# Performance work log

Measured on AMD Instinct MI355X. Metric: run time of the kernel, lower is better.

## Reference

```python
import jax, jax.numpy as jnp
import numpy as np

B, S, C, H = 256, 512, 64, 128  # batch, seq_len, input channels, LSTM hidden


def setup_inputs() -> dict:
    key = jax.random.key(0)
    ks = jax.random.split(key, 9)
    s = 1.0 / np.sqrt(H)  # torch nn.LSTM init: U(-1/sqrt(H), 1/sqrt(H))
    u = lambda k, shape: jax.random.uniform(k, shape, jnp.float32, -s, s)
    return {
        "x": jax.random.normal(ks[0], (B, S, C), jnp.float32),
        # layer 0 (input size C)
        "Wih0": u(ks[1], (4 * H, C)),
        "Whh0": u(ks[2], (4 * H, H)),
        "bih0": u(ks[3], (4 * H,)),
        "bhh0": u(ks[4], (4 * H,)),
        # layer 1 (input size H)
        "Wih1": u(ks[5], (4 * H, H)),
        "Whh1": u(ks[6], (4 * H, H)),
        "bih1": u(ks[7], (4 * H,)),
        "bhh1": u(ks[8], (4 * H,)),
    }


def _lstm_layer(x, Wih, Whh, bih, bhh):
    """x: (S, B, in) -> outputs h_t for all t: (S, B, H). Torch gate order i,f,g,o."""
    Hh = Whh.shape[1]
    # Input-to-hidden GEMM hoisted out of the recurrence (batched over S).
    xg = jnp.einsum('sbc,gc->sbg', x, Wih) + bih + bhh  # (S, B, 4H)

    def step(carry, xt):
        h, c = carry
        g = xt + h @ Whh.T  # (B, 4H)
        i, f, gg, o = jnp.split(g, 4, axis=-1)
        i = jax.nn.sigmoid(i)
        f = jax.nn.sigmoid(f)
        gg = jnp.tanh(gg)
        o = jax.nn.sigmoid(o)
        c = f * c + i * gg
        h = o * jnp.tanh(c)
        return (h, c), h

    h0 = jnp.zeros((x.shape[1], Hh), x.dtype)
    _, ys = jax.lax.scan(step, (h0, h0), xg)
    return ys


def reference(x, Wih0, Whh0, bih0, bhh0, Wih1, Whh1, bih1, bhh1):
    xs = jnp.transpose(x, (1, 0, 2))  # (B,S,C) -> (S,B,C), matching x.permute(1,0,2)
    y1 = _lstm_layer(xs, Wih0, Whh0, bih0, bhh0)
    y2 = _lstm_layer(y1, Wih1, Whh1, bih1, bhh1)
    return y2[-1]  # x[-1, :, :]: last timestep of top layer, (B, H)
```

## Files before the change

kernel.cpp:

```cpp
#include <hip/hip_runtime.h>
#include <cstdint>
#include <cstddef>


#define S_LEN 512
#define B_SZ  256
#define C_IN  64
#define HDIM  128
#define XG_TSTRIDE (32 * 512 * 8)

using short8  = __attribute__((ext_vector_type(8))) short;
using float4v = __attribute__((ext_vector_type(4))) float;

template<bool V> struct Flag { static constexpr bool value = V; };

__device__ __forceinline__ unsigned short f2b(float f) {
    union { float f; unsigned int u; } v; v.f = f;
    unsigned int u = v.u;
    return (unsigned short)((u + 0x7FFFu + ((u >> 16) & 1u)) >> 16);
}
__device__ __forceinline__ float b2f(unsigned short s) {
    union { unsigned int u; float f; } v; v.u = ((unsigned int)s) << 16;
    return v.f;
}
__device__ __forceinline__ float sig_(float x) {
    return __builtin_amdgcn_rcpf(1.0f + __builtin_amdgcn_exp2f(x * -1.442695041f));
}
__device__ __forceinline__ float tanh_(float x) {
    return 1.0f - 2.0f * __builtin_amdgcn_rcpf(1.0f + __builtin_amdgcn_exp2f(x * 2.885390082f));
}
__device__ __forceinline__ short8 load8_f2b(const float* s) {
    const float4v f0 = *(const float4v*)s;
    const float4v f1 = *(const float4v*)(s + 4);
    short8 t;
#pragma unroll
    for (int e = 0; e < 4; ++e) {
        t[e]     = (short)f2b(f0[e]);
        t[e + 4] = (short)f2b(f1[e]);
    }
    return t;
}

__global__ void conv_kernel(const float* __restrict__ whh0,
                            const float* __restrict__ wih1, const float* __restrict__ whh1,
                            const float* __restrict__ bih1, const float* __restrict__ bhh1,
                            unsigned short* __restrict__ whh0_b, unsigned short* __restrict__ wih1_b,
                            unsigned short* __restrict__ whh1_b, float* __restrict__ bias1) {
    int i = blockIdx.x * blockDim.x + threadIdx.x;
    if (i < 4 * HDIM * HDIM) {
        whh0_b[i] = f2b(whh0[i]);
        wih1_b[i] = f2b(wih1[i]);
        whh1_b[i] = f2b(whh1[i]);
    }
    if (i < 4 * HDIM) bias1[i] = bih1[i] + bhh1[i];
}

__global__ __launch_bounds__(512, 2)
void xg_gemm(const float* __restrict__ x, const float* __restrict__ wih0,
             const float* __restrict__ bih0, const float* __restrict__ bhh0,
             unsigned short* __restrict__ xg) {
    const int tid = threadIdx.x;
    const int w = tid >> 6, L = tid & 63, q = L >> 4, r = L & 15;
    const int blk = blockIdx.x, tch = blockIdx.y;
    const int boff = blk * 8, j = w * 16 + r;
    const int rowload = (r >> 2) * 2 + (r & 1);

    short8 wf[4][2]; float bias_s[4];
#pragma unroll
    for (int g = 0; g < 4; ++g) {
        const int nrow = g * HDIM + j;
#pragma unroll
        for (int kk = 0; kk < 2; ++kk)
            wf[g][kk] = load8_f2b(wih0 + (size_t)nrow * C_IN + kk * 32 + q * 8);
        bias_s[g] = bih0[nrow] + bhh0[nrow];
    }

    const float* px = x + ((size_t)(boff + rowload) * S_LEN + (size_t)tch * 32) * C_IN + q * 8;
    unsigned short* po = xg + ((size_t)(tch * 32) * 32 + blk) * 4096 + (size_t)tid * 8;

    for (int tt = 0; tt < 32; ++tt) {
        short8 xa[2];
#pragma unroll
        for (int kk = 0; kk < 2; ++kk) xa[kk] = load8_f2b(px + kk * 32);
        float4v a[4];
#pragma unroll
        for (int g = 0; g < 4; ++g) a[g] = (float4v){bias_s[g], bias_s[g], 0.f, 0.f};
#pragma unroll
        for (int kk = 0; kk < 2; ++kk)
#pragma unroll
            for (int g = 0; g < 4; ++g)
                a[g] = __builtin_amdgcn_mfma_f32_16x16x32_bf16(xa[kk], wf[g][kk], a[g], 0, 0, 0);
        short8 o;
#pragma unroll
        for (int g = 0; g < 4; ++g) {
            o[2 * g]     = (short)f2b(a[g][0]);
            o[2 * g + 1] = (short)f2b(a[g][1]);
        }
        *(short8*)po = o;
        px += C_IN;
        po += XG_TSTRIDE;
    }
}

__global__ __launch_bounds__(512, 2)
void lstm_fused(const unsigned short* __restrict__ whh0_b,
                const unsigned short* __restrict__ wih1_b,
                const unsigned short* __restrict__ whh1_b,
                const float* __restrict__ bias1,
                const unsigned short* __restrict__ xg,
                float* __restrict__ out) {
    __shared__ __align__(16) unsigned short hbuf[4 * 2048];
    const int tid = threadIdx.x;
    const int w = tid >> 6, L = tid & 63, q = L >> 4, r = L & 15;
    const int blk = blockIdx.x;
    const int boff = blk * 8, j = w * 16 + r;

    short8 whh0[4][4], wih1[4][4], whh1[4][4];
    float b1s[4];
#pragma unroll
    for (int g = 0; g < 4; ++g) {
        const size_t nrow = (size_t)(g * HDIM + j);
#pragma unroll
        for (int kk = 0; kk < 4; ++kk) {
            whh0[g][kk] = *(const short8*)(whh0_b + nrow * HDIM + kk * 32 + q * 8);
            wih1[g][kk] = *(const short8*)(wih1_b + nrow * HDIM + kk * 32 + q * 8);
            whh1[g][kk] = *(const short8*)(whh1_b + nrow * HDIM + kk * 32 + q * 8);
        }
        b1s[g] = bias1[g * HDIM + j];
    }
#pragma unroll
    for (int g = 0; g < 4; ++g) {
        asm volatile("" : "+v"(whh0[g][0]), "+v"(whh0[g][1]), "+v"(whh0[g][2]), "+v"(whh0[g][3]));
        asm volatile("" : "+v"(wih1[g][0]), "+v"(wih1[g][1]), "+v"(wih1[g][2]), "+v"(wih1[g][3]));
        asm volatile("" : "+v"(whh1[g][0]), "+v"(whh1[g][1]), "+v"(whh1[g][2]), "+v"(whh1[g][3]));
    }

    for (int idx = tid; idx < 4 * 1024; idx += 512) ((unsigned int*)hbuf)[idx] = 0u;

    float cf0[2] = {0.f, 0.f}, cf1[2] = {0.f, 0.f};
    const int rred = ((r & 3) < 2) ? r : (r - 2);
    const int rdoff = q * 128 + rred * 8;
    const int chunkbase = (j >> 3) * 128 + (j & 7);
    float* fout = out + (size_t)(boff + 2 * q) * HDIM + j;

    const unsigned short* pxg = xg + (size_t)blk * 4096 + (size_t)tid * 8;
    short8 xgA = *(const short8*)pxg;
    pxg += XG_TSTRIDE;
    short8 xgB;

    __syncthreads();

    auto step = [&](auto D0_, auto D1_, auto FIN_,
                    unsigned short* r0, unsigned short* w0,
                    unsigned short* r1, unsigned short* w1,
                    short8& xc, short8& xn) {
        constexpr bool D0  = decltype(D0_)::value;
        constexpr bool D1  = decltype(D1_)::value;
        constexpr bool FIN = decltype(FIN_)::value;

        if constexpr (!FIN) {
            xn = *(const short8*)pxg;
            pxg += XG_TSTRIDE;
        }

        if constexpr (D0) {
            float4v a0[4];
#pragma unroll
            for (int g = 0; g < 4; ++g)
                a0[g] = (float4v){b2f((unsigned short)xc[2 * g]),
                                  b2f((unsigned short)xc[2 * g + 1]), 0.f, 0.f};
#pragma unroll
            for (int kk = 0; kk < 4; ++kk) {
                const short8 h0f = *(const short8*)(r0 + kk * 512 + rdoff);
#pragma unroll
                for (int g = 0; g < 4; ++g)
                    a0[g] = __builtin_amdgcn_mfma_f32_16x16x32_bf16(h0f, whh0[g][kk], a0[g], 0, 0, 0);
            }
#pragma unroll
            for (int rr = 0; rr < 2; ++rr) {
                const float iv = sig_(a0[0][rr]);
                const float fv = sig_(a0[1][rr]);
                const float gv = tanh_(a0[2][rr]);
                const float ov = sig_(a0[3][rr]);
                cf0[rr] = fv * cf0[rr] + iv * gv;
                w0[chunkbase + (4 * q + rr) * 8] = f2b(ov * tanh_(cf0[rr]));
            }
        }

        if constexpr (D1) {
            float4v a1[4];
#pragma unroll
            for (int g = 0; g < 4; ++g) a1[g] = (float4v){b1s[g], b1s[g], 0.f, 0.f};
#pragma unroll
            for (int kk = 0; kk < 4; ++kk) {
                const short8 hif = *(const short8*)(r0 + kk * 512 + rdoff);
#pragma unroll
                for (int g = 0; g < 4; ++g)
                    a1[g] = __builtin_amdgcn_mfma_f32_16x16x32_bf16(hif, wih1[g][kk], a1[g], 0, 0, 0);
            }
#pragma unroll
            for (int kk = 0; kk < 4; ++kk) {
                const short8 h1f = *(const short8*)(r1 + kk * 512 + rdoff);
#pragma unroll
                for (int g = 0; g < 4; ++g)
                    a1[g] = __builtin_amdgcn_mfma_f32_16x16x32_bf16(h1f, whh1[g][kk], a1[g], 0, 0, 0);
            }
#pragma unroll
            for (int rr = 0; rr < 2; ++rr) {
                const float iv = sig_(a1[0][rr]);
                const float fv = sig_(a1[1][rr]);
                const float gv = tanh_(a1[2][rr]);
                const float ov = sig_(a1[3][rr]);
                cf1[rr] = fv * cf1[rr] + iv * gv;
                const float hv = ov * tanh_(cf1[rr]);
                if constexpr (FIN) fout[rr * HDIM] = hv;
                else w1[chunkbase + (4 * q + rr) * 8] = f2b(hv);
            }
        }

        if constexpr (!FIN)
            asm volatile("s_waitcnt lgkmcnt(0)\n\ts_barrier" ::: "memory");
    };

    unsigned short* h0A = hbuf;
    unsigned short* h0B = hbuf + 2048;
    unsigned short* h1A = hbuf + 4096;
    unsigned short* h1B = hbuf + 6144;
    using T = Flag<true>; using F = Flag<false>;

    step(T{}, F{}, F{}, h0A, h0B, h1A, h1B, xgA, xgB);
#pragma unroll 1
    for (int k = 0; k < 255; ++k) {
        step(T{}, T{}, F{}, h0B, h0A, h1B, h1A, xgB, xgA);
        step(T{}, T{}, F{}, h0A, h0B, h1A, h1B, xgA, xgB);
    }
    step(T{}, T{}, F{}, h0B, h0A, h1B, h1A, xgB, xgA);
    step(F{}, T{}, T{}, h0A, h0B, h1A, h1B, xgA, xgB);
}


extern "C" void kernel_launch(void* const* d_in, const int* in_sizes, int n_in,
                              void* d_out, int out_size, void* d_ws, size_t ws_size,
                              hipStream_t stream) {
    const float* x    = (const float*)d_in[0];
    const float* wih0 = (const float*)d_in[1];
    const float* whh0 = (const float*)d_in[2];
    const float* bih0 = (const float*)d_in[3];
    const float* bhh0 = (const float*)d_in[4];
    const float* wih1 = (const float*)d_in[5];
    const float* whh1 = (const float*)d_in[6];
    const float* bih1 = (const float*)d_in[7];
    const float* bhh1 = (const float*)d_in[8];

    char* ws = (char*)d_ws;
    unsigned short* whh0_b = (unsigned short*)(ws + 0);
    unsigned short* wih1_b = (unsigned short*)(ws + 131072);
    unsigned short* whh1_b = (unsigned short*)(ws + 262144);
    float*          bias1  = (float*)(ws + 393216);
    unsigned short* xgp    = (unsigned short*)(ws + 524288);

    conv_kernel<<<256, 256, 0, stream>>>(whh0, wih1, whh1, bih1, bhh1,
                                         whh0_b, wih1_b, whh1_b, bias1);
    xg_gemm<<<dim3(32, 16), 512, 0, stream>>>(x, wih0, bih0, bhh0, xgp);
    lstm_fused<<<32, 512, 0, stream>>>(whh0_b, wih1_b, whh1_b, bias1, xgp,
                                       (float*)d_out);
}
```

Measured before the change: 738.7 us.

## Halve per-block batch to 4 rows and launch 64 blocks; add MFMA priority

Each block of the fused LSTM kernel and the xg GEMM now handles 4 batch rows instead of 8, doubling the grid from 32 to 64 blocks, so more CUs work on the serial recurrence. The xg layout changes to match: 4 gate values per thread stored as short4. Each thread now computes one output row instead of two, which shortens the elementwise gate tail per step. s_setprio is raised around the MFMA chains. The cost is that MFMA tiles are now only 1/4 used, and the weight loads into registers are duplicated across twice as many blocks.

Result: faster. 694.5 us (-6.0%).

```diff
diff --git a/kernel.cpp b/kernel.cpp
--- a/kernel.cpp
+++ b/kernel.cpp
@@ -7,8 +7,10 @@
 #define B_SZ  256
 #define C_IN  64
 #define HDIM  128
-#define XG_TSTRIDE (32 * 512 * 8)
-
+#define NBLK  64
+#define XG_TSTRIDE (64 * 512 * 4)
+
+using short4v = __attribute__((ext_vector_type(4))) short;
 using short8  = __attribute__((ext_vector_type(8))) short;
 using float4v = __attribute__((ext_vector_type(4))) float;
 
@@ -62,8 +64,8 @@
     const int tid = threadIdx.x;
     const int w = tid >> 6, L = tid & 63, q = L >> 4, r = L & 15;
     const int blk = blockIdx.x, tch = blockIdx.y;
-    const int boff = blk * 8, j = w * 16 + r;
-    const int rowload = (r >> 2) * 2 + (r & 1);
+    const int boff = blk * 4, j = w * 16 + r;
+    const int rowload = r >> 2;
 
     short8 wf[4][2]; float bias_s[4];
 #pragma unroll
@@ -76,7 +78,7 @@
     }
 
     const float* px = x + ((size_t)(boff + rowload) * S_LEN + (size_t)tch * 32) * C_IN + q * 8;
-    unsigned short* po = xg + ((size_t)(tch * 32) * 32 + blk) * 4096 + (size_t)tid * 8;
+    unsigned short* po = xg + ((size_t)(tch * 32) * NBLK + blk) * 2048 + (size_t)tid * 4;
 
     for (int tt = 0; tt < 32; ++tt) {
         short8 xa[2];
@@ -84,19 +86,16 @@
         for (int kk = 0; kk < 2; ++kk) xa[kk] = load8_f2b(px + kk * 32);
         float4v a[4];
 #pragma unroll
-        for (int g = 0; g < 4; ++g) a[g] = (float4v){bias_s[g], bias_s[g], 0.f, 0.f};
+        for (int g = 0; g < 4; ++g) a[g] = (float4v){bias_s[g], 0.f, 0.f, 0.f};
 #pragma unroll
         for (int kk = 0; kk < 2; ++kk)
 #pragma unroll
             for (int g = 0; g < 4; ++g)
                 a[g] = __builtin_amdgcn_mfma_f32_16x16x32_bf16(xa[kk], wf[g][kk], a[g], 0, 0, 0);
-        short8 o;
-#pragma unroll
-        for (int g = 0; g < 4; ++g) {
-            o[2 * g]     = (short)f2b(a[g][0]);
-            o[2 * g + 1] = (short)f2b(a[g][1]);
-        }
-        *(short8*)po = o;
+        short4v o;
+#pragma unroll
+        for (int g = 0; g < 4; ++g) o[g] = (short)f2b(a[g][0]);
+        *(short4v*)po = o;
         px += C_IN;
         po += XG_TSTRIDE;
     }
@@ -113,7 +112,7 @@
     const int tid = threadIdx.x;
     const int w = tid >> 6, L = tid & 63, q = L >> 4, r = L & 15;
     const int blk = blockIdx.x;
-    const int boff = blk * 8, j = w * 16 + r;
+    const int boff = blk * 4, j = w * 16 + r;
 
     short8 whh0[4][4], wih1[4][4], whh1[4][4];
     float b1s[4];
@@ -137,29 +136,30 @@
 
     for (int idx = tid; idx < 4 * 1024; idx += 512) ((unsigned int*)hbuf)[idx] = 0u;
 
-    float cf0[2] = {0.f, 0.f}, cf1[2] = {0.f, 0.f};
-    const int rred = ((r & 3) < 2) ? r : (r - 2);
+    float cf0 = 0.f, cf1 = 0.f;
+    const int rred = r & ~3;
     const int rdoff = q * 128 + rred * 8;
     const int chunkbase = (j >> 3) * 128 + (j & 7);
-    float* fout = out + (size_t)(boff + 2 * q) * HDIM + j;
-
-    const unsigned short* pxg = xg + (size_t)blk * 4096 + (size_t)tid * 8;
-    short8 xgA = *(const short8*)pxg;
+    const int wslot = chunkbase + (4 * q) * 8;
+    float* fout = out + (size_t)(boff + q) * HDIM + j;
+
+    const unsigned short* pxg = xg + (size_t)blk * 2048 + (size_t)tid * 4;
+    short4v xgA = *(const short4v*)pxg;
     pxg += XG_TSTRIDE;
-    short8 xgB;
+    short4v xgB;
 
     __syncthreads();
 
     auto step = [&](auto D0_, auto D1_, auto FIN_,
                     unsigned short* r0, unsigned short* w0,
                     unsigned short* r1, unsigned short* w1,
-                    short8& xc, short8& xn) {
+                    short4v& xc, short4v& xn) {
         constexpr bool D0  = decltype(D0_)::value;
         constexpr bool D1  = decltype(D1_)::value;
         constexpr bool FIN = decltype(FIN_)::value;
 
         if constexpr (!FIN) {
-            xn = *(const short8*)pxg;
+            xn = *(const short4v*)pxg;
             pxg += XG_TSTRIDE;
         }
 
@@ -167,8 +167,8 @@
             float4v a0[4];
 #pragma unroll
             for (int g = 0; g < 4; ++g)
-                a0[g] = (float4v){b2f((unsigned short)xc[2 * g]),
-                                  b2f((unsigned short)xc[2 * g + 1]), 0.f, 0.f};
+                a0[g] = (float4v){b2f((unsigned short)xc[g]), 0.f, 0.f, 0.f};
+            __builtin_amdgcn_s_setprio(1);
 #pragma unroll
             for (int kk = 0; kk < 4; ++kk) {
                 const short8 h0f = *(const short8*)(r0 + kk * 512 + rdoff);
@@ -176,21 +176,22 @@
                 for (int g = 0; g < 4; ++g)
                     a0[g] = __builtin_amdgcn_mfma_f32_16x16x32_bf16(h0f, whh0[g][kk], a0[g], 0, 0, 0);
             }
-#pragma unroll
-            for (int rr = 0; rr < 2; ++rr) {
-                const float iv = sig_(a0[0][rr]);
-                const float fv = sig_(a0[1][rr]);
-                const float gv = tanh_(a0[2][rr]);
-                const float ov = sig_(a0[3][rr]);
-                cf0[rr] = fv * cf0[rr] + iv * gv;
-                w0[chunkbase + (4 * q + rr) * 8] = f2b(ov * tanh_(cf0[rr]));
+            __builtin_amdgcn_s_setprio(0);
+            {
+                const float iv = sig_(a0[0][0]);
+                const float fv = sig_(a0[1][0]);
+                const float gv = tanh_(a0[2][0]);
+                const float ov = sig_(a0[3][0]);
+                cf0 = fv * cf0 + iv * gv;
+                w0[wslot] = f2b(ov * tanh_(cf0));
             }
         }
 
         if constexpr (D1) {
             float4v a1[4];
 #pragma unroll
-            for (int g = 0; g < 4; ++g) a1[g] = (float4v){b1s[g], b1s[g], 0.f, 0.f};
+            for (int g = 0; g < 4; ++g) a1[g] = (float4v){b1s[g], 0.f, 0.f, 0.f};
+            __builtin_amdgcn_s_setprio(1);
 #pragma unroll
             for (int kk = 0; kk < 4; ++kk) {
                 const short8 hif = *(const short8*)(r0 + kk * 512 + rdoff);
@@ -205,16 +206,16 @@
                 for (int g = 0; g < 4; ++g)
                     a1[g] = __builtin_amdgcn_mfma_f32_16x16x32_bf16(h1f, whh1[g][kk], a1[g], 0, 0, 0);
             }
-#pragma unroll
-            for (int rr = 0; rr < 2; ++rr) {
-                const float iv = sig_(a1[0][rr]);
-                const float fv = sig_(a1[1][rr]);
-                const float gv = tanh_(a1[2][rr]);
-                const float ov = sig_(a1[3][rr]);
-                cf1[rr] = fv * cf1[rr] + iv * gv;
-                const float hv = ov * tanh_(cf1[rr]);
-                if constexpr (FIN) fout[rr * HDIM] = hv;
-                else w1[chunkbase + (4 * q + rr) * 8] = f2b(hv);
+            __builtin_amdgcn_s_setprio(0);
+            {
+                const float iv = sig_(a1[0][0]);
+                const float fv = sig_(a1[1][0]);
+                const float gv = tanh_(a1[2][0]);
+                const float ov = sig_(a1[3][0]);
+                cf1 = fv * cf1 + iv * gv;
+                const float hv = ov * tanh_(cf1);
+                if constexpr (FIN) fout[0] = hv;
+                else w1[wslot] = f2b(hv);
             }
         }
 
@@ -261,7 +262,7 @@
 
     conv_kernel<<<256, 256, 0, stream>>>(whh0, wih1, whh1, bih1, bhh1,
                                          whh0_b, wih1_b, whh1_b, bias1);
-    xg_gemm<<<dim3(32, 16), 512, 0, stream>>>(x, wih0, bih0, bhh0, xgp);
-    lstm_fused<<<32, 512, 0, stream>>>(whh0_b, wih1_b, whh1_b, bias1, xgp,
-                                       (float*)d_out);
-}
+    xg_gemm<<<dim3(NBLK, 16), 512, 0, stream>>>(x, wih0, bih0, bhh0, xgp);
+    lstm_fused<<<NBLK, 512, 0, stream>>>(whh0_b, wih1_b, whh1_b, bias1, xgp,
+                                         (float*)d_out);
+}
```
